# Kernel tuning notes

Measured on AMD Instinct MI355X. Metric: run time of the kernel, lower is better.

Reference implementation:

```python
import jax, jax.numpy as jnp
import numpy as np

NUM_BUCKETS = 32
MAX_DISTANCE = 128
NUM_HEADS = 16
D_KV = 64


def _relative_position_bucket(relative_position):
    # bidirectional buckets, faithful to T5Attention._relative_position_bucket
    num_buckets = NUM_BUCKETS // 2
    relative_buckets = (relative_position > 0).astype(jnp.int32) * num_buckets
    relative_position = jnp.abs(relative_position)
    max_exact = num_buckets // 2
    is_small = relative_position < max_exact
    rp_f = relative_position.astype(jnp.float32)
    rel_if_large = max_exact + (
        jnp.log(rp_f / max_exact) / np.log(MAX_DISTANCE / max_exact) * (num_buckets - max_exact)
    )
    rel_if_large = jnp.minimum(rel_if_large, num_buckets - 1)
    relative_buckets = relative_buckets + jnp.where(is_small, rp_f, rel_if_large).astype(jnp.int32)
    return relative_buckets


def setup_inputs() -> dict:
    key = jax.random.key(0)
    ks = jax.random.split(key, 6)
    B, S, D = 2, 2048, 1024
    inner = NUM_HEADS * D_KV  # 1024
    q_std = (inner * D_KV) ** (-0.5)
    kv_std = inner ** (-0.5)
    return {
        "hidden_states": jax.random.normal(ks[0], (B, S, D), jnp.float32),
        "attention_mask": jnp.ones((B, S), jnp.int32),
        "Wq": jax.random.normal(ks[1], (D, inner), jnp.float32) * q_std,
        "Wk": jax.random.normal(ks[2], (D, inner), jnp.float32) * kv_std,
        "Wv": jax.random.normal(ks[3], (D, inner), jnp.float32) * kv_std,
        "Wo": jax.random.normal(ks[4], (inner, D), jnp.float32) * kv_std,
        "rel_bias": jax.random.normal(ks[5], (NUM_BUCKETS, NUM_HEADS), jnp.float32),
    }


def reference(hidden_states, attention_mask, Wq, Wk, Wv, Wo, rel_bias):
    B, S, D = hidden_states.shape
    H, Dk = NUM_HEADS, D_KV

    q = (hidden_states @ Wq).reshape(B, S, H, Dk)
    k = (hidden_states @ Wk).reshape(B, S, H, Dk)
    v = (hidden_states @ Wv).reshape(B, S, H, Dk)
    q = q / jnp.sqrt(jnp.asarray(Dk, q.dtype))

    scores = jnp.einsum('bthd,bshd->bhts', q, k)  # [B,H,S,S]

    # relative position bias
    pos = jnp.arange(S, dtype=jnp.int32)
    rel_pos = pos[None, :] - pos[:, None]          # memory - context, [S,S]
    buckets = _relative_position_bucket(rel_pos)   # [S,S]
    bias = rel_bias[buckets]                       # [S,S,H]
    scores = scores + bias.transpose(2, 0, 1)[None].astype(scores.dtype)

    mask = attention_mask[:, None, None, :].astype(scores.dtype)
    scores = scores + (1.0 - mask) * jnp.finfo(scores.dtype).min

    attn = jax.nn.softmax(scores, axis=-1)
    out = jnp.einsum('bhts,bshd->bthd', attn, v).reshape(B, S, H * Dk)
    return out @ Wo
```

## Files before the change

kernel.cpp:

```cpp
#include <hip/hip_runtime.h>
#include <hip/hip_bf16.h>
#include <math.h>

typedef __attribute__((ext_vector_type(8))) short bf16x8;
typedef __attribute__((ext_vector_type(4))) short s16x4;
typedef __attribute__((ext_vector_type(4))) float f32x4;

constexpr int cB = 2, cS = 2048, cH = 16, cD = 64, cIn = 1024, cM = 1024;

union BfPack { bf16x8 v; short s[8]; };
union BfPack4 { s16x4 v; short s[4]; };

__device__ __forceinline__ short f2bf(float f) {
    union { float f; unsigned u; } v; v.f = f;
    unsigned r = v.u + 0x7fffu + ((v.u >> 16) & 1u);
    return (short)(r >> 16);
}

__device__ __forceinline__ f32x4 mfma16(bf16x8 a, bf16x8 b, f32x4 c) {
    return __builtin_amdgcn_mfma_f32_16x16x32_bf16(a, b, c, 0, 0, 0);
}

__device__ __forceinline__ void async16(const short* g, short* l) {
    __builtin_amdgcn_global_load_lds(
        (const __attribute__((address_space(1))) unsigned*)(uintptr_t)g,
        (__attribute__((address_space(3))) unsigned*)(uintptr_t)l, 16, 0, 0);
}

__global__ void bias_table_kernel(const float* __restrict__ rel_bias,
                                  const int* __restrict__ mask,
                                  float* __restrict__ bt,
                                  float* __restrict__ maskadd) {
    int idx = blockIdx.x * blockDim.x + threadIdx.x;
    if (idx < 4096) maskadd[idx] = (1.0f - (float)mask[idx]) * -3.0e38f;
    if (idx >= 4095) return;
    int delta = idx - 2047;
    int rb = (delta > 0) ? 16 : 0;
    int ar = delta < 0 ? -delta : delta;
    int bucket;
    if (ar < 8) {
        bucket = rb + ar;
    } else {
        float rl = 8.0f + logf((float)ar * 0.125f) * 2.8853900817779268f;
        rl = fminf(rl, 15.0f);
        bucket = rb + (int)rl;
    }
    #pragma unroll
    for (int h = 0; h < cH; h++)
        bt[h * 4096 + 2048 + delta] = rel_bias[bucket * cH + h];
}

__global__ __launch_bounds__(256) void conv_hidden_kernel(
    const float* __restrict__ h, short* __restrict__ hbf) {
    int t = blockIdx.x * 256 + threadIdx.x;
    const float4* src = (const float4*)h;
    float4 a = src[2 * t], b = src[2 * t + 1];
    BfPack p;
    p.s[0] = f2bf(a.x); p.s[1] = f2bf(a.y); p.s[2] = f2bf(a.z); p.s[3] = f2bf(a.w);
    p.s[4] = f2bf(b.x); p.s[5] = f2bf(b.y); p.s[6] = f2bf(b.z); p.s[7] = f2bf(b.w);
    ((bf16x8*)hbf)[t] = p.v;
}

__global__ __launch_bounds__(256) void conv_wt_kernel(
    const float* __restrict__ Wq, const float* __restrict__ Wk,
    const float* __restrict__ Wv, const float* __restrict__ Wo,
    short* __restrict__ Wt) {
    const int z = blockIdx.z;
    const float* W = (z == 0) ? Wq : (z == 1) ? Wk : (z == 2) ? Wv : Wo;
    const float scale = (z == 0) ? 0.125f : 1.0f;
    const int n0 = blockIdx.x * 64, k0 = blockIdx.y * 64;
    __shared__ short sW[64][72];
    const int t = threadIdx.x;
    const int r = t >> 2, c4 = (t & 3) * 16;
    {
        const float* src = W + (size_t)(k0 + r) * cM + n0 + c4;
        BfPack p[2];
        #pragma unroll
        for (int q = 0; q < 2; q++) {
            float4 x = ((const float4*)src)[2 * q];
            float4 y = ((const float4*)src)[2 * q + 1];
            p[q].s[0] = f2bf(x.x * scale); p[q].s[1] = f2bf(x.y * scale);
            p[q].s[2] = f2bf(x.z * scale); p[q].s[3] = f2bf(x.w * scale);
            p[q].s[4] = f2bf(y.x * scale); p[q].s[5] = f2bf(y.y * scale);
            p[q].s[6] = f2bf(y.z * scale); p[q].s[7] = f2bf(y.w * scale);
        }
        *(bf16x8*)&sW[r][c4] = p[0].v;
        *(bf16x8*)&sW[r][c4 + 8] = p[1].v;
    }
    __syncthreads();
    const int n = t >> 2, kc = (t & 3) * 16;
    BfPack o0, o1;
    #pragma unroll
    for (int j = 0; j < 8; j++) o0.s[j] = sW[kc + j][n];
    #pragma unroll
    for (int j = 0; j < 8; j++) o1.s[j] = sW[kc + 8 + j][n];
    short* dst = Wt + (size_t)z * cM * cIn + (size_t)(n0 + n) * cIn + k0 + kc;
    *(bf16x8*)dst = o0.v;
    *(bf16x8*)(dst + 8) = o1.v;
}

template <bool SWAP>
__device__ __forceinline__ void gemm_core(
    const short* __restrict__ A, const short* __restrict__ Bt,
    short* smem, int m0, int c0, int tid, f32x4 (&acc)[4][4]) {
    short* sA = smem;
    short* sB = smem + 4096;
    const int w = tid >> 6, l = tid & 63;
    const int m16 = l & 15, g = l >> 4;
    const int srow = l >> 2, scol = (l & 3) * 8;
    const int mq = (w & 1) * 64, nq = (w >> 1) * 64;

    for (int k0 = 0; k0 < cIn; k0 += 32) {
        __syncthreads();
        async16(A + (size_t)(m0 + w * 16 + srow) * cIn + k0 + scol,
                sA + w * 512 + l * 8);
        async16(A + (size_t)(m0 + 64 + w * 16 + srow) * cIn + k0 + scol,
                sA + 2048 + w * 512 + l * 8);
        async16(Bt + (size_t)(c0 + w * 16 + srow) * cIn + k0 + scol,
                sB + w * 512 + l * 8);
        async16(Bt + (size_t)(c0 + 64 + w * 16 + srow) * cIn + k0 + scol,
                sB + 2048 + w * 512 + l * 8);
        __syncthreads();
        bf16x8 af[4], bf[4];
        #pragma unroll
        for (int i = 0; i < 4; i++)
            af[i] = *(const bf16x8*)(sA + (mq + i * 16 + m16) * 32 + g * 8);
        #pragma unroll
        for (int j = 0; j < 4; j++)
            bf[j] = *(const bf16x8*)(sB + (nq + j * 16 + m16) * 32 + g * 8);
        #pragma unroll
        for (int i = 0; i < 4; i++)
            #pragma unroll
            for (int j = 0; j < 4; j++)
                acc[i][j] = SWAP ? mfma16(bf[j], af[i], acc[i][j])
                                 : mfma16(af[i], bf[j], acc[i][j]);
    }
}

__global__ __launch_bounds__(256) void gemm_qkv_kernel(
    const short* __restrict__ hbf, const short* __restrict__ Wt,
    short* __restrict__ Qrm, short* __restrict__ Krm, short* __restrict__ VT) {
    const int z = blockIdx.z;
    const short* Bt = Wt + (size_t)z * cM * cIn;
    const int m0 = blockIdx.y * 128, c0 = blockIdx.x * 128;
    __shared__ short smem[8192];
    const int tid = threadIdx.x, w = tid >> 6, l = tid & 63;
    const int m16 = l & 15, g = l >> 4;
    const int mq = (w & 1) * 64, nq = (w >> 1) * 64;
    f32x4 acc[4][4] = {};

    if (z <= 1) {
        gemm_core<false>(hbf, Bt, smem, m0, c0, tid, acc);
        short* dst = (z == 0) ? Qrm : Krm;
        #pragma unroll
        for (int i = 0; i < 4; i++)
            #pragma unroll
            for (int j = 0; j < 4; j++)
                #pragma unroll
                for (int r = 0; r < 4; r++)
                    dst[(size_t)(m0 + mq + i * 16 + g * 4 + r) * cM +
                        c0 + nq + j * 16 + m16] = f2bf(acc[i][j][r]);
    } else {
        gemm_core<true>(hbf, Bt, smem, m0, c0, tid, acc);
        #pragma unroll
        for (int i = 0; i < 4; i++) {
            const int srow_g = m0 + mq + i * 16 + m16;
            const int bb = srow_g >> 11, ss = srow_g & 2047;
            #pragma unroll
            for (int j = 0; j < 4; j++)
                #pragma unroll
                for (int r = 0; r < 4; r++) {
                    const int wcol = c0 + nq + j * 16 + g * 4 + r;
                    VT[(((size_t)bb * cH + (wcol >> 6)) * cD + (wcol & 63)) * cS
                       + ss] = f2bf(acc[i][j][r]);
                }
        }
    }
}

__global__ __launch_bounds__(256) void attn_kernel(
    const short* __restrict__ Qrm, const short* __restrict__ Krm,
    const short* __restrict__ VT, const float* __restrict__ maskadd,
    const float* __restrict__ bias_t, short* __restrict__ ctx) {
    const int b = blockIdx.z, h = blockIdx.y;
    const int q0 = blockIdx.x * 64;
    const short* VTp = VT + ((size_t)b * cH + h) * cS * cD;
    const float* bh = bias_t + h * 4096 + 2048;
    const float* mp = maskadd + b * cS;

    const int tid = threadIdx.x;
    const int wave = tid >> 6, lane = tid & 63;
    const int m16 = lane & 15, g = lane >> 4;

    __shared__ short Kt[64][72];
    __shared__ short Vt[64][72];

    const int q = q0 + wave * 16 + m16;
    const short* qb = Qrm + (size_t)(b * cS + q) * cM + h * cD;
    bf16x8 qf0 = *(const bf16x8*)(qb + g * 8);
    bf16x8 qf1 = *(const bf16x8*)(qb + 32 + g * 8);

    f32x4 o[4] = {};
    float lsum = 0.f;

    const int srow = tid >> 3;
    const int scol = (tid & 7) << 3;
    const int kb = ((scol >> 4) & 1) * 32 + ((scol >> 3) & 1) * 16 +
                   ((scol >> 5) & 1) * 4;
    const short* kbase = Krm + (size_t)b * cS * cM + h * cD;

    for (int kt = 0; kt < cS; kt += 64) {
        __syncthreads();
        *(bf16x8*)&Kt[srow][scol] =
            *(const bf16x8*)(kbase + (size_t)(kt + srow) * cM + scol);
        *(bf16x8*)&Kt[srow + 32][scol] =
            *(const bf16x8*)(kbase + (size_t)(kt + srow + 32) * cM + scol);
        {
            BfPack v0, v1;
            v0.v = *(const bf16x8*)(VTp + (size_t)srow * cS + kt + scol);
            v1.v = *(const bf16x8*)(VTp + (size_t)(srow + 32) * cS + kt + scol);
            BfPack4 a, bb2, c, d;
            #pragma unroll
            for (int i = 0; i < 4; i++) { a.s[i] = v0.s[i]; bb2.s[i] = v0.s[4 + i]; }
            #pragma unroll
            for (int i = 0; i < 4; i++) { c.s[i] = v1.s[i]; d.s[i] = v1.s[4 + i]; }
            *(s16x4*)&Vt[srow][kb]          = a.v;
            *(s16x4*)&Vt[srow][kb + 8]      = bb2.v;
            *(s16x4*)&Vt[srow + 32][kb]     = c.v;
            *(s16x4*)&Vt[srow + 32][kb + 8] = d.v;
        }
        __syncthreads();

        f32x4 s[4];
        #pragma unroll
        for (int st = 0; st < 4; st++) {
            bf16x8 klo = *(const bf16x8*)&Kt[st * 16 + m16][g * 8];
            bf16x8 khi = *(const bf16x8*)&Kt[st * 16 + m16][32 + g * 8];
            f32x4 t = {};
            t = mfma16(klo, qf0, t);
            t = mfma16(khi, qf1, t);
            s[st] = t;
        }

        BfPack pp[2];
        #pragma unroll
        for (int st = 0; st < 4; st++) {
            const int keybase = kt + st * 16 + g * 4;
            #pragma unroll
            for (int r = 0; r < 2; r++) {
                float x0 = s[st][2 * r] + bh[keybase + 2 * r - q] + mp[keybase + 2 * r];
                float x1 = s[st][2 * r + 1] + bh[keybase + 2 * r + 1 - q] + mp[keybase + 2 * r + 1];
                float p0 = __expf(x0), p1 = __expf(x1);
                lsum += p0 + p1;
                __hip_bfloat162 h2 = __float22bfloat162_rn(float2{p0, p1});
                short2 sp = *(short2*)&h2;
                pp[st & 1].s[(st >> 1) * 4 + 2 * r]     = sp.x;
                pp[st & 1].s[(st >> 1) * 4 + 2 * r + 1] = sp.y;
            }
        }

        #pragma unroll
        for (int nt = 0; nt < 4; nt++) {
            bf16x8 vlo = *(const bf16x8*)&Vt[nt * 16 + m16][g * 8];
            bf16x8 vhi = *(const bf16x8*)&Vt[nt * 16 + m16][32 + g * 8];
            o[nt] = mfma16(vlo, pp[0].v, o[nt]);
            o[nt] = mfma16(vhi, pp[1].v, o[nt]);
        }
    }

    lsum += __shfl_xor(lsum, 16, 64);
    lsum += __shfl_xor(lsum, 32, 64);
    const float inv = 1.0f / lsum;

    short* cb = ctx + ((size_t)b * cS + q) * cM + h * cD;
    #pragma unroll
    for (int nt = 0; nt < 4; nt++) {
        BfPack4 pk;
        #pragma unroll
        for (int r = 0; r < 4; r++) pk.s[r] = f2bf(o[nt][r] * inv);
        *(s16x4*)(cb + nt * 16 + g * 4) = pk.v;
    }
}

__global__ __launch_bounds__(256) void gemm_o_kernel(
    const short* __restrict__ ctx, const short* __restrict__ WoT,
    float* __restrict__ out) {
    const int m0 = blockIdx.y * 128, c0 = blockIdx.x * 128;
    __shared__ short smem[8192];
    const int tid = threadIdx.x, w = tid >> 6, l = tid & 63;
    const int m16 = l & 15, g = l >> 4;
    const int mq = (w & 1) * 64, nq = (w >> 1) * 64;
    f32x4 acc[4][4] = {};
    gemm_core<false>(ctx, WoT, smem, m0, c0, tid, acc);
    #pragma unroll
    for (int i = 0; i < 4; i++)
        #pragma unroll
        for (int j = 0; j < 4; j++)
            #pragma unroll
            for (int r = 0; r < 4; r++)
                out[(size_t)(m0 + mq + i * 16 + g * 4 + r) * cM +
                    c0 + nq + j * 16 + m16] = acc[i][j][r];
}

extern "C" void kernel_launch(void* const* d_in, const int* in_sizes, int n_in,
                              void* d_out, int out_size, void* d_ws, size_t ws_size,
                              hipStream_t stream) {
    const float* hidden   = (const float*)d_in[0];
    const int*   mask     = (const int*)d_in[1];
    const float* Wq       = (const float*)d_in[2];
    const float* Wk       = (const float*)d_in[3];
    const float* Wv       = (const float*)d_in[4];
    const float* Wo       = (const float*)d_in[5];
    const float* rel_bias = (const float*)d_in[6];
    float* out = (float*)d_out;

    short* hbf_ctx = (short*)d_ws;
    short* Wt  = hbf_ctx + (size_t)4 * 1024 * 1024;
    short* Qrm = Wt  + (size_t)4 * 1024 * 1024;
    short* Krm = Qrm + (size_t)4 * 1024 * 1024;
    short* VT  = Krm + (size_t)4 * 1024 * 1024;
    float* bias_t  = (float*)(VT + (size_t)4 * 1024 * 1024);
    float* maskf   = bias_t + 16 * 4096;

    bias_table_kernel<<<16, 256, 0, stream>>>(rel_bias, mask, bias_t, maskf);
    conv_hidden_kernel<<<2048, 256, 0, stream>>>(hidden, hbf_ctx);
    conv_wt_kernel<<<dim3(16, 16, 4), 256, 0, stream>>>(Wq, Wk, Wv, Wo, Wt);
    gemm_qkv_kernel<<<dim3(8, 32, 3), 256, 0, stream>>>(hbf_ctx, Wt, Qrm, Krm, VT);
    attn_kernel<<<dim3(32, cH, cB), 256, 0, stream>>>(Qrm, Krm, VT, maskf, bias_t,
                                                      hbf_ctx);
    gemm_o_kernel<<<dim3(8, 32), 256, 0, stream>>>(hbf_ctx, Wt + (size_t)3 * 1024 * 1024,
                                                   out);
}
```

Before: 216.3 us.

## Prefetch K/V tiles into registers, use exp2, fold bias into MFMA init, MFMA row sums

In the attention kernel, the next K/V tile is now loaded from global memory into registers while the current tile is being computed, so load latency overlaps with math. The log2(e) factor is folded into the Q weight scale and the relative-bias table, which lets the kernel use the hardware exp2 instead of __expf. Bias and mask are fed in as the MFMA accumulator initial value, removing separate adds after the matmul. The softmax denominator is computed by an MFMA against a ones vector, replacing the scalar sums and cross-lane shuffles. In exchange the kernel uses more registers, and the row sum is now taken from bf16-rounded probabilities.

```diff
diff --git a/kernel.cpp b/kernel.cpp
--- a/kernel.cpp
+++ b/kernel.cpp
@@ -7,6 +7,7 @@
 typedef __attribute__((ext_vector_type(4))) float f32x4;
 
 constexpr int cB = 2, cS = 2048, cH = 16, cD = 64, cIn = 1024, cM = 1024;
+constexpr float cLog2e = 1.4426950408889634f;
 
 union BfPack { bf16x8 v; short s[8]; };
 union BfPack4 { s16x4 v; short s[4]; };
@@ -47,7 +48,7 @@
     }
     #pragma unroll
     for (int h = 0; h < cH; h++)
-        bt[h * 4096 + 2048 + delta] = rel_bias[bucket * cH + h];
+        bt[h * 4096 + 2048 + delta] = rel_bias[bucket * cH + h] * cLog2e;
 }
 
 __global__ __launch_bounds__(256) void conv_hidden_kernel(
@@ -67,7 +68,7 @@
     short* __restrict__ Wt) {
     const int z = blockIdx.z;
     const float* W = (z == 0) ? Wq : (z == 1) ? Wk : (z == 2) ? Wv : Wo;
-    const float scale = (z == 0) ? 0.125f : 1.0f;
+    const float scale = (z == 0) ? 0.125f * cLog2e : 1.0f;
     const int n0 = blockIdx.x * 64, k0 = blockIdx.y * 64;
     __shared__ short sW[64][72];
     const int t = threadIdx.x;
@@ -201,7 +202,10 @@
     bf16x8 qf1 = *(const bf16x8*)(qb + 32 + g * 8);
 
     f32x4 o[4] = {};
-    float lsum = 0.f;
+    f32x4 lacc = {};
+    BfPack ones;
+    #pragma unroll
+    for (int i = 0; i < 8; i++) ones.s[i] = (short)0x3F80;
 
     const int srow = tid >> 3;
     const int scol = (tid & 7) << 3;
@@ -209,49 +213,55 @@
                    ((scol >> 5) & 1) * 4;
     const short* kbase = Krm + (size_t)b * cS * cM + h * cD;
 
+    bf16x8 kr0 = *(const bf16x8*)(kbase + (size_t)srow * cM + scol);
+    bf16x8 kr1 = *(const bf16x8*)(kbase + (size_t)(srow + 32) * cM + scol);
+    bf16x8 vr0 = *(const bf16x8*)(VTp + (size_t)srow * cS + scol);
+    bf16x8 vr1 = *(const bf16x8*)(VTp + (size_t)(srow + 32) * cS + scol);
+
     for (int kt = 0; kt < cS; kt += 64) {
         __syncthreads();
-        *(bf16x8*)&Kt[srow][scol] =
-            *(const bf16x8*)(kbase + (size_t)(kt + srow) * cM + scol);
-        *(bf16x8*)&Kt[srow + 32][scol] =
-            *(const bf16x8*)(kbase + (size_t)(kt + srow + 32) * cM + scol);
+        *(bf16x8*)&Kt[srow][scol] = kr0;
+        *(bf16x8*)&Kt[srow + 32][scol] = kr1;
         {
-            BfPack v0, v1;
-            v0.v = *(const bf16x8*)(VTp + (size_t)srow * cS + kt + scol);
-            v1.v = *(const bf16x8*)(VTp + (size_t)(srow + 32) * cS + kt + scol);
-            BfPack4 a, bb2, c, d;
-            #pragma unroll
-            for (int i = 0; i < 4; i++) { a.s[i] = v0.s[i]; bb2.s[i] = v0.s[4 + i]; }
+            BfPack v0, v1; v0.v = vr0; v1.v = vr1;
+            BfPack4 a, b2, c, d;
+            #pragma unroll
+            for (int i = 0; i < 4; i++) { a.s[i] = v0.s[i]; b2.s[i] = v0.s[4 + i]; }
             #pragma unroll
             for (int i = 0; i < 4; i++) { c.s[i] = v1.s[i]; d.s[i] = v1.s[4 + i]; }
             *(s16x4*)&Vt[srow][kb]          = a.v;
-            *(s16x4*)&Vt[srow][kb + 8]      = bb2.v;
+            *(s16x4*)&Vt[srow][kb + 8]      = b2.v;
             *(s16x4*)&Vt[srow + 32][kb]     = c.v;
             *(s16x4*)&Vt[srow + 32][kb + 8] = d.v;
         }
         __syncthreads();
 
+        const int ktn = (kt + 64 < cS) ? kt + 64 : 0;
+        kr0 = *(const bf16x8*)(kbase + (size_t)(ktn + srow) * cM + scol);
+        kr1 = *(const bf16x8*)(kbase + (size_t)(ktn + srow + 32) * cM + scol);
+        vr0 = *(const bf16x8*)(VTp + (size_t)srow * cS + ktn + scol);
+        vr1 = *(const bf16x8*)(VTp + (size_t)(srow + 32) * cS + ktn + scol);
+
         f32x4 s[4];
         #pragma unroll
         for (int st = 0; st < 4; st++) {
+            const int keyb = kt + st * 16 + g * 4;
+            f32x4 init;
+            #pragma unroll
+            for (int c = 0; c < 4; c++)
+                init[c] = bh[keyb + c - q] + mp[keyb + c];
             bf16x8 klo = *(const bf16x8*)&Kt[st * 16 + m16][g * 8];
             bf16x8 khi = *(const bf16x8*)&Kt[st * 16 + m16][32 + g * 8];
-            f32x4 t = {};
-            t = mfma16(klo, qf0, t);
-            t = mfma16(khi, qf1, t);
-            s[st] = t;
+            s[st] = mfma16(khi, qf1, mfma16(klo, qf0, init));
         }
 
         BfPack pp[2];
         #pragma unroll
         for (int st = 0; st < 4; st++) {
-            const int keybase = kt + st * 16 + g * 4;
             #pragma unroll
             for (int r = 0; r < 2; r++) {
-                float x0 = s[st][2 * r] + bh[keybase + 2 * r - q] + mp[keybase + 2 * r];
-                float x1 = s[st][2 * r + 1] + bh[keybase + 2 * r + 1 - q] + mp[keybase + 2 * r + 1];
-                float p0 = __expf(x0), p1 = __expf(x1);
-                lsum += p0 + p1;
+                float p0 = __builtin_amdgcn_exp2f(s[st][2 * r]);
+                float p1 = __builtin_amdgcn_exp2f(s[st][2 * r + 1]);
                 __hip_bfloat162 h2 = __float22bfloat162_rn(float2{p0, p1});
                 short2 sp = *(short2*)&h2;
                 pp[st & 1].s[(st >> 1) * 4 + 2 * r]     = sp.x;
@@ -259,6 +269,9 @@
             }
         }
 
+        lacc = mfma16(ones.v, pp[0].v, lacc);
+        lacc = mfma16(ones.v, pp[1].v, lacc);
+
         #pragma unroll
         for (int nt = 0; nt < 4; nt++) {
             bf16x8 vlo = *(const bf16x8*)&Vt[nt * 16 + m16][g * 8];
@@ -268,10 +281,7 @@
         }
     }
 
-    lsum += __shfl_xor(lsum, 16, 64);
-    lsum += __shfl_xor(lsum, 32, 64);
-    const float inv = 1.0f / lsum;
-
+    const float inv = 1.0f / lacc[0];
     short* cb = ctx + ((size_t)b * cS + q) * cM + h * cD;
     #pragma unroll
     for (int nt = 0; nt < 4; nt++) {
```

After: 213.8 us. No clear change (-1.2%).
